# Kernel optimization log

Hardware: AMD Instinct MI355X
Metric: run time of the kernel (lower is better)

The kernel has to match this reference:

```python
import jax, jax.numpy as jnp
import numpy as np

WD, WH, WW = 1, 7, 7
N = WD * WH * WW  # 49 tokens per window
LN_EPS = 1e-5


def _make_rel_coords_table():
    rd = np.arange(-(WD - 1), WD, dtype=np.float32)
    rh = np.arange(-(WH - 1), WH, dtype=np.float32)
    rw = np.arange(-(WW - 1), WW, dtype=np.float32)
    g = np.stack(np.meshgrid(rd, rh, rw, indexing='ij'), axis=-1)  # (2wd-1,2wh-1,2ww-1,3)
    eps = 1e-6
    g = g / (np.array([WD, WH, WW], np.float32) - (1.0 - eps))
    g = g * 8.0
    g = np.sign(g) * np.log2(np.abs(g) + 1.0) / np.log2(8.0)
    return g[None].astype(np.float32)  # (1,2wd-1,2wh-1,2ww-1,3)


def _make_rel_pos_index():
    coords = np.stack(np.meshgrid(np.arange(WD), np.arange(WH), np.arange(WW), indexing='ij'))
    cf = coords.reshape(3, -1)  # (3,N)
    rel = cf[:, :, None] - cf[:, None, :]  # (3,N,N)
    rel = rel.transpose(1, 2, 0).astype(np.int64)
    rel[..., 0] += WD - 1
    rel[..., 1] += WH - 1
    rel[..., 2] += WW - 1
    rel[..., 0] *= (2 * WH - 1) * (2 * WW - 1)
    rel[..., 1] *= 2 * WW - 1
    return rel.sum(-1).astype(np.int32)  # (N,N)


def setup_inputs() -> dict:
    key = jax.random.key(0)
    ks = jax.random.split(key, 8)
    B, D, H, W, C = 4, 8, 56, 56, 256
    nh, hid = 8, 4 * C

    def init_w(k, shape, fan_in):
        return (jax.random.normal(k, shape, jnp.float32) / np.sqrt(fan_in)).astype(jnp.float32)

    inp = {
        'x': jax.random.normal(ks[0], (B, D, H, W, C), jnp.float32),
        'qkv_w': init_w(ks[1], (3 * C, C), C),
        'q_bias': jnp.zeros((C,), jnp.float32),
        'v_bias': jnp.zeros((C,), jnp.float32),
        'logit_scale': jnp.full((nh, 1, 1), np.log(10.0), jnp.float32),
        'cpb_w1': init_w(ks[2], (512, 3), 3),
        'cpb_b1': jnp.zeros((512,), jnp.float32),
        'cpb_w2': init_w(ks[3], (nh, 512), 512),
        'proj_w': init_w(ks[4], (C, C), C),
        'proj_b': jnp.zeros((C,), jnp.float32),
        'norm1_g': jnp.ones((C,), jnp.float32),
        'norm1_b': jnp.zeros((C,), jnp.float32),
        'fc1_w': init_w(ks[5], (hid, C), C),
        'fc1_b': jnp.zeros((hid,), jnp.float32),
        'fc2_w': init_w(ks[6], (C, hid), hid),
        'fc2_b': jnp.zeros((C,), jnp.float32),
        'norm2_g': jnp.ones((C,), jnp.float32),
        'norm2_b': jnp.zeros((C,), jnp.float32),
        'rel_coords_table': jnp.asarray(_make_rel_coords_table()),
        'rel_pos_index': jnp.asarray(_make_rel_pos_index()),
    }
    return inp


def _layernorm(x, g, b):
    mu = jnp.mean(x, axis=-1, keepdims=True)
    var = jnp.mean(jnp.square(x - mu), axis=-1, keepdims=True)
    return (x - mu) * jax.lax.rsqrt(var + LN_EPS) * g + b


def _l2norm(x):
    # F.normalize(dim=-1): x / max(||x||, 1e-12)
    n = jnp.sqrt(jnp.sum(jnp.square(x), axis=-1, keepdims=True))
    return x / jnp.maximum(n, 1e-12)


def _forward(x, qkv_w, q_bias, v_bias, logit_scale, cpb_w1, cpb_b1, cpb_w2,
             proj_w, proj_b, norm1_g, norm1_b, fc1_w, fc1_b, fc2_w, fc2_b,
             norm2_g, norm2_b, rel_coords_table, rel_pos_index):
    B, D, H, W, C = x.shape
    nh = logit_scale.shape[0]
    hd = C // nh

    # ---- window partition: (B,D,H,W,C) -> (B_, N, C)
    xw = x.reshape(B, D // WD, WD, H // WH, WH, W // WW, WW, C)
    xw = xw.transpose(0, 1, 3, 5, 2, 4, 6, 7).reshape(-1, N, C)
    Bw = xw.shape[0]

    # ---- qkv with (q_bias, 0, v_bias)
    qkv_bias = jnp.concatenate([q_bias, jnp.zeros_like(q_bias), v_bias])
    qkv = xw @ qkv_w.T + qkv_bias  # (Bw,N,3C)
    qkv = qkv.reshape(Bw, N, 3, nh, hd).transpose(2, 0, 3, 1, 4)
    q, k, v = qkv[0], qkv[1], qkv[2]  # (Bw,nh,N,hd)

    # ---- cosine attention with clamped learned logit scale
    attn = jnp.einsum('bhnd,bhmd->bhnm', _l2norm(q), _l2norm(k))
    scale = jnp.exp(jnp.minimum(logit_scale, jnp.float32(np.log(100.0))))  # (nh,1,1)
    attn = attn * scale

    # ---- CPB-MLP relative position bias
    t = rel_coords_table.reshape(-1, 3)
    hcpb = jax.nn.relu(t @ cpb_w1.T + cpb_b1)
    table = hcpb @ cpb_w2.T  # (T, nh)
    rpb = table[rel_pos_index.reshape(-1)].reshape(N, N, nh).transpose(2, 0, 1)
    rpb = 16.0 * jax.nn.sigmoid(rpb)
    attn = attn + rpb[None]

    attn = jax.nn.softmax(attn, axis=-1)
    out = jnp.einsum('bhnm,bhmd->bhnd', attn, v)
    out = out.transpose(0, 2, 1, 3).reshape(Bw, N, C)
    out = out @ proj_w.T + proj_b

    # ---- window reverse
    xr = out.reshape(B, D // WD, H // WH, W // WW, WD, WH, WW, C)
    xr = xr.transpose(0, 1, 4, 2, 5, 3, 6, 7).reshape(B, D, H, W, C)

    # ---- Swin-v2 post-norm residuals
    x = x + _layernorm(xr, norm1_g, norm1_b)
    h = jax.nn.gelu(x @ fc1_w.T + fc1_b, approximate=False)
    y = h @ fc2_w.T + fc2_b
    x = x + _layernorm(y, norm2_g, norm2_b)
    return x


def reference(x, qkv_w, q_bias, v_bias, logit_scale, cpb_w1, cpb_b1, cpb_w2,
              proj_w, proj_b, norm1_g, norm1_b, fc1_w, fc1_b, fc2_w, fc2_b,
              norm2_g, norm2_b, rel_coords_table, rel_pos_index):
    return _forward(x, qkv_w, q_bias, v_bias, logit_scale, cpb_w1, cpb_b1, cpb_w2,
                    proj_w, proj_b, norm1_g, norm1_b, fc1_w, fc1_b, fc2_w, fc2_b,
                    norm2_g, norm2_b, rel_coords_table, rel_pos_index)
```

## Files before the change

kernel.cpp:

```cpp
#include <hip/hip_runtime.h>
#include <hip/hip_bf16.h>

typedef __attribute__((ext_vector_type(8))) short short8_t;
typedef __attribute__((ext_vector_type(4))) float f32x4;

__device__ __forceinline__ float bf2f(unsigned short u) {
    return __uint_as_float(((unsigned)u) << 16);
}
__device__ __forceinline__ unsigned short f2bf(float f) {
    __hip_bfloat16 h = __float2bfloat16(f);
    return *reinterpret_cast<unsigned short*>(&h);
}

__device__ __forceinline__ float fast_gelu(float v) {
    float ax = fabsf(v) * 0.70710678118f;
    float t  = __builtin_amdgcn_rcpf(1.f + 0.3275911f * ax);
    float poly = t * (0.254829592f + t * (-0.284496736f + t * (1.421413741f
               + t * (-1.453152027f + t * 1.061405429f))));
    float e  = __expf(-ax * ax);
    float er = 1.f - poly * e;
    float s  = (v >= 0.f) ? er : -er;
    return 0.5f * v * (1.f + s);
}

__device__ __forceinline__ void async16(const unsigned short* g, unsigned short* l) {
    __builtin_amdgcn_global_load_lds(
        (const __attribute__((address_space(1))) unsigned int*)g,
        (__attribute__((address_space(3))) unsigned int*)l,
        16, 0, 0);
}

__device__ __forceinline__ int win_row_to_token(int r) {
    int wb = r / 49, n = r - wb * 49;
    int wq = wb & 7, hb = (wb >> 3) & 7, d = (wb >> 6) & 7, b = wb >> 9;
    int hh = n / 7, ww2 = n - hh * 7;
    return ((b * 8 + d) * 56 + hb * 7 + hh) * 56 + wq * 7 + ww2;
}

__global__ __launch_bounds__(256) void conv_kernel(
    const float* __restrict__ src, unsigned short* __restrict__ dst, int n4)
{
    int stride = gridDim.x * 256;
    for (int i = blockIdx.x * 256 + threadIdx.x; i < n4; i += stride) {
        float4 v = *reinterpret_cast<const float4*>(&src[(size_t)i * 4]);
        short4 o;
        o.x = (short)f2bf(v.x); o.y = (short)f2bf(v.y);
        o.z = (short)f2bf(v.z); o.w = (short)f2bf(v.w);
        *reinterpret_cast<short4*>(&dst[(size_t)i * 4]) = o;
    }
}

__global__ __launch_bounds__(256) void conv4_kernel(
    const float* __restrict__ s0, unsigned short* __restrict__ d0, int n0,
    const float* __restrict__ s1, unsigned short* __restrict__ d1, int n1,
    const float* __restrict__ s2, unsigned short* __restrict__ d2, int n2,
    const float* __restrict__ s3, unsigned short* __restrict__ d3, int n3)
{
    int stride = gridDim.x * 256;
    int total = n0 + n1 + n2 + n3;
    for (int i = blockIdx.x * 256 + threadIdx.x; i < total; i += stride) {
        const float* s; unsigned short* d; int j = i;
        if (j < n0) { s = s0; d = d0; }
        else if ((j -= n0) < n1) { s = s1; d = d1; }
        else if ((j -= n1) < n2) { s = s2; d = d2; }
        else { j -= n2; s = s3; d = d3; }
        float4 v = *reinterpret_cast<const float4*>(&s[(size_t)j * 4]);
        short4 o;
        o.x = (short)f2bf(v.x); o.y = (short)f2bf(v.y);
        o.z = (short)f2bf(v.z); o.w = (short)f2bf(v.w);
        *reinterpret_cast<short4*>(&d[(size_t)j * 4]) = o;
    }
}

__global__ __launch_bounds__(256) void prep_table_kernel(
    const float* __restrict__ w1, const float* __restrict__ b1,
    const float* __restrict__ w2, const float* __restrict__ tabin,
    float* __restrict__ tableg)
{
    const int i = blockIdx.x;
    const int t = threadIdx.x;
    const float c0 = tabin[i * 3], c1 = tabin[i * 3 + 1], c2 = tabin[i * 3 + 2];
    float part[8] = {0.f, 0.f, 0.f, 0.f, 0.f, 0.f, 0.f, 0.f};
    for (int j = t; j < 512; j += 256) {
        float hv = fmaxf(c0 * w1[j * 3] + c1 * w1[j * 3 + 1] + c2 * w1[j * 3 + 2] + b1[j], 0.f);
        #pragma unroll
        for (int h = 0; h < 8; ++h) part[h] += hv * w2[h * 512 + j];
    }
    #pragma unroll
    for (int h = 0; h < 8; ++h) {
        float v = part[h];
        v += __shfl_xor(v, 1);  v += __shfl_xor(v, 2);  v += __shfl_xor(v, 4);
        v += __shfl_xor(v, 8);  v += __shfl_xor(v, 16); v += __shfl_xor(v, 32);
        part[h] = v;
    }
    __shared__ float red[4][8];
    const int wv = t >> 6, lane = t & 63;
    if (lane == 0) {
        #pragma unroll
        for (int h = 0; h < 8; ++h) red[wv][h] = part[h];
    }
    __syncthreads();
    if (t < 8) tableg[i * 8 + t] = red[0][t] + red[1][t] + red[2][t] + red[3][t];
}

__global__ __launch_bounds__(256) void prep_expand_kernel(
    const float* __restrict__ logit_scale,
    const float* __restrict__ qb, const float* __restrict__ vb,
    const int* __restrict__ rpi, const float* __restrict__ tableg,
    float* __restrict__ scales, float* __restrict__ rpbf,
    float* __restrict__ qkvb)
{
    const int stride = gridDim.x * 256;
    const int gt = blockIdx.x * 256 + threadIdx.x;
    if (gt < 8) scales[gt] = expf(fminf(logit_scale[gt], 4.6051702f));
    for (int i = gt; i < 768; i += stride) {
        float o;
        if (i < 256) o = qb[i];
        else if (i < 512) o = 0.f;
        else o = vb[i - 512];
        qkvb[i] = o;
    }
    for (int e = gt; e < 32768; e += stride) {
        int h = e >> 12, rem = e & 4095;
        int mi = rem >> 10, ji = (rem >> 8) & 3;
        int r16 = (rem >> 4) & 15, g4 = (rem >> 2) & 3, r = rem & 3;
        int i = mi * 16 + g4 * 4 + r, j = ji * 16 + r16;
        float val = 0.f;
        if (i < 49 && j < 49) {
            float xv = tableg[rpi[i * 49 + j] * 8 + h];
            val = 16.f / (1.f + expf(-xv));
        }
        rpbf[e] = val;
    }
}

template<int ACT>
__global__ __launch_bounds__(512, 6) void gemm2_kernel(
    const unsigned short* __restrict__ A, const unsigned short* __restrict__ W,
    const float* __restrict__ bias, unsigned short* __restrict__ C,
    int M, int N, int K, int ntn)
{
    __shared__ unsigned short smem[24576];
    const int tid = threadIdx.x;
    const int lane = tid & 63, wv = tid >> 6;
    const int wr = wv >> 2, wc = wv & 3;
    const int nwg = gridDim.x;
    const int virt = (blockIdx.x & 7) * (nwg >> 3) + (blockIdx.x >> 3);
    const int bn = virt % ntn, bm = virt / ntn;
    const size_t arow0 = (size_t)bm * 128;
    const size_t brow0 = (size_t)bn * 128;
    const int r16 = lane & 15, g4 = lane >> 4;
    const int srow_l = lane >> 2;
    const int sgran  = (lane & 3) ^ ((srow_l >> 1) & 3);
    f32x4 acc[4][2] = {};

    auto STAGE = [&](int buf, int kt) {
        unsigned short* As = smem + buf * 8192;
        unsigned short* Bs = As + 4096;
        int row0 = wv * 16;
        async16(&A[(arow0 + row0 + srow_l) * (size_t)K + kt + sgran * 8], &As[row0 * 32]);
        async16(&W[(brow0 + row0 + srow_l) * (size_t)K + kt + sgran * 8], &Bs[row0 * 32]);
    };
    auto COMPUTE = [&](int buf) {
        unsigned short* As = smem + buf * 8192;
        unsigned short* Bs = As + 4096;
        short8_t af[4], bfr[2];
        const int gsw = g4 ^ ((r16 >> 1) & 3);
        #pragma unroll
        for (int m = 0; m < 4; ++m) {
            int row = wr * 64 + m * 16 + r16;
            af[m] = *reinterpret_cast<const short8_t*>(&As[row * 32 + gsw * 8]);
        }
        #pragma unroll
        for (int n = 0; n < 2; ++n) {
            int row = wc * 32 + n * 16 + r16;
            bfr[n] = *reinterpret_cast<const short8_t*>(&Bs[row * 32 + gsw * 8]);
        }
        #pragma unroll
        for (int m = 0; m < 4; ++m)
            #pragma unroll
            for (int n = 0; n < 2; ++n)
                acc[m][n] = __builtin_amdgcn_mfma_f32_16x16x32_bf16(af[m], bfr[n], acc[m][n], 0, 0, 0);
    };

    const int nk = K >> 5;
    STAGE(0, 0);
    STAGE(1, 32);
    int cb = 0;
    for (int ks = 0; ks < nk; ++ks) {
        if (ks == nk - 1) { asm volatile("s_waitcnt vmcnt(0)" ::: "memory"); }
        else              { asm volatile("s_waitcnt vmcnt(2)" ::: "memory"); }
        __builtin_amdgcn_sched_barrier(0);
        asm volatile("s_barrier" ::: "memory");
        if (ks + 2 < nk) {
            int sb = cb + 2; if (sb >= 3) sb -= 3;
            STAGE(sb, (ks + 2) << 5);
        }
        __builtin_amdgcn_sched_barrier(0);
        COMPUTE(cb);
        cb = (cb == 2) ? 0 : cb + 1;
    }
    __builtin_amdgcn_sched_barrier(0);
    asm volatile("s_barrier" ::: "memory");

    unsigned short* Cs = smem + wv * 2304;
    const int rbase = g4 * 4;
    const int srow = lane >> 2, scol = (lane & 3) * 8;
    const int gcol0 = bn * 128 + wc * 32;
    #pragma unroll
    for (int n = 0; n < 2; ++n) {
        float bv = bias[gcol0 + n * 16 + r16];
        #pragma unroll
        for (int m = 0; m < 4; ++m)
            #pragma unroll
            for (int r = 0; r < 4; ++r) {
                float v = acc[m][n][r] + bv;
                if (ACT == 1) v = fast_gelu(v);
                Cs[(m * 16 + rbase + r) * 36 + n * 16 + r16] = f2bf(v);
            }
    }
    #pragma unroll
    for (int pass = 0; pass < 4; ++pass) {
        int lr = pass * 16 + srow;
        int grow = bm * 128 + wr * 64 + lr;
        short8_t vv = *reinterpret_cast<const short8_t*>(&Cs[lr * 36 + scol]);
        *reinterpret_cast<short8_t*>(&C[(size_t)grow * N + gcol0 + scol]) = vv;
    }
}

template<int SCATTER, int OUT_F32>
__global__ __launch_bounds__(512) void gemm_ln_kernel(
    const unsigned short* __restrict__ A, const unsigned short* __restrict__ W,
    const float* __restrict__ bias, const unsigned short* __restrict__ resid,
    const float* __restrict__ gamma, const float* __restrict__ beta,
    void* __restrict__ Cv, int M, int K)
{
    __shared__ unsigned short smem[36864];
    const int tid = threadIdx.x;
    const int lane = tid & 63, wv = tid >> 6;
    const int wr = wv >> 2, wc = wv & 3;
    const int nwg = gridDim.x;
    const int bm = (blockIdx.x & 7) * (nwg >> 3) + (blockIdx.x >> 3);
    const size_t arow0 = (size_t)bm * 128;
    const int r16 = lane & 15, g4 = lane >> 4;
    const int srow_l = lane >> 2;
    const int sgran = (lane & 3) ^ ((srow_l >> 1) & 3);
    f32x4 acc[4][4] = {};

    auto STAGE = [&](int buf, int kt) {
        unsigned short* As = smem + buf * 12288;
        unsigned short* Bs = As + 4096;
        async16(&A[(arow0 + wv * 16 + srow_l) * (size_t)K + kt + sgran * 8],
                &As[(wv * 16) * 32]);
        #pragma unroll
        for (int i = 0; i < 2; ++i) {
            int row0 = wv * 32 + i * 16;
            async16(&W[(size_t)(row0 + srow_l) * K + kt + sgran * 8], &Bs[row0 * 32]);
        }
    };
    auto COMPUTE = [&](int buf) {
        unsigned short* As = smem + buf * 12288;
        unsigned short* Bs = As + 4096;
        short8_t af[4], bfr[4];
        const int gsw = g4 ^ ((r16 >> 1) & 3);
        #pragma unroll
        for (int m = 0; m < 4; ++m) {
            int row = wr * 64 + m * 16 + r16;
            af[m] = *reinterpret_cast<const short8_t*>(&As[row * 32 + gsw * 8]);
        }
        #pragma unroll
        for (int n = 0; n < 4; ++n) {
            int row = wc * 64 + n * 16 + r16;
            bfr[n] = *reinterpret_cast<const short8_t*>(&Bs[row * 32 + gsw * 8]);
        }
        #pragma unroll
        for (int m = 0; m < 4; ++m)
            #pragma unroll
            for (int n = 0; n < 4; ++n)
                acc[m][n] = __builtin_amdgcn_mfma_f32_16x16x32_bf16(af[m], bfr[n], acc[m][n], 0, 0, 0);
    };

    const int nk = K >> 5;
    STAGE(0, 0);
    STAGE(1, 32);
    int cb = 0;
    for (int ks = 0; ks < nk; ++ks) {
        if (ks == nk - 1) { asm volatile("s_waitcnt vmcnt(0)" ::: "memory"); }
        else              { asm volatile("s_waitcnt vmcnt(3)" ::: "memory"); }
        __builtin_amdgcn_sched_barrier(0);
        asm volatile("s_barrier" ::: "memory");
        if (ks + 2 < nk) {
            int sb = cb + 2; if (sb >= 3) sb -= 3;
            STAGE(sb, (ks + 2) << 5);
        }
        __builtin_amdgcn_sched_barrier(0);
        COMPUTE(cb);
        cb = (cb == 2) ? 0 : cb + 1;
    }
    __builtin_amdgcn_sched_barrier(0);
    asm volatile("s_barrier" ::: "memory");

    float bv[4];
    #pragma unroll
    for (int n = 0; n < 4; ++n) bv[n] = bias[wc * 64 + n * 16 + r16];
    float* psum  = reinterpret_cast<float*>(smem + 19456);
    float* psq   = psum + 512;
    float* stats = psq + 512;
    #pragma unroll
    for (int m = 0; m < 4; ++m) {
        #pragma unroll
        for (int r = 0; r < 4; ++r) {
            float s = 0.f, s2 = 0.f;
            #pragma unroll
            for (int n = 0; n < 4; ++n) {
                float v = acc[m][n][r] + bv[n];
                s += v; s2 += v * v;
            }
            s  += __shfl_xor(s, 1);  s  += __shfl_xor(s, 2);
            s  += __shfl_xor(s, 4);  s  += __shfl_xor(s, 8);
            s2 += __shfl_xor(s2, 1); s2 += __shfl_xor(s2, 2);
            s2 += __shfl_xor(s2, 4); s2 += __shfl_xor(s2, 8);
            if (r16 == 0) {
                int row = wr * 64 + m * 16 + g4 * 4 + r;
                psum[row * 4 + wc] = s;
                psq[row * 4 + wc]  = s2;
            }
        }
    }
    __syncthreads();
    if (tid < 128) {
        f32x4 a = *reinterpret_cast<const f32x4*>(&psum[tid * 4]);
        f32x4 b = *reinterpret_cast<const f32x4*>(&psq[tid * 4]);
        float mu  = (a[0] + a[1] + a[2] + a[3]) * 0.00390625f;
        float ex2 = (b[0] + b[1] + b[2] + b[3]) * 0.00390625f;
        stats[tid * 2]     = mu;
        stats[tid * 2 + 1] = rsqrtf(ex2 - mu * mu + 1e-5f);
    }
    __syncthreads();

    unsigned short* Cs = smem + wv * 2432;
    const int rbase = g4 * 4;
    const int srow = lane >> 3, scol = (lane & 7) * 8;
    const int gcol0 = wc * 64;
    f32x4 gm0 = *reinterpret_cast<const f32x4*>(&gamma[gcol0 + scol]);
    f32x4 gm1 = *reinterpret_cast<const f32x4*>(&gamma[gcol0 + scol + 4]);
    f32x4 bt0 = *reinterpret_cast<const f32x4*>(&beta[gcol0 + scol]);
    f32x4 bt1 = *reinterpret_cast<const f32x4*>(&beta[gcol0 + scol + 4]);
    #pragma unroll
    for (int p = 0; p < 2; ++p) {
        #pragma unroll
        for (int n = 0; n < 4; ++n)
            #pragma unroll
            for (int m2 = 0; m2 < 2; ++m2)
                #pragma unroll
                for (int r = 0; r < 4; ++r)
                    Cs[(m2 * 16 + rbase + r) * 76 + n * 16 + r16] =
                        f2bf(acc[p * 2 + m2][n][r] + bv[n]);
        #pragma unroll
        for (int rr = 0; rr < 4; ++rr) {
            int lr = rr * 8 + srow;
            int lrow = wr * 64 + p * 32 + lr;
            int grow = bm * 128 + lrow;
            size_t orow = SCATTER ? (size_t)win_row_to_token(grow) : (size_t)grow;
            float mu  = stats[lrow * 2];
            float inv = stats[lrow * 2 + 1];
            short8_t cv = *reinterpret_cast<const short8_t*>(&Cs[lr * 76 + scol]);
            short8_t rv = *reinterpret_cast<const short8_t*>(&resid[orow * 256 + gcol0 + scol]);
            float o[8];
            #pragma unroll
            for (int e = 0; e < 8; ++e) {
                float g = (e < 4) ? gm0[e] : gm1[e - 4];
                float bb = (e < 4) ? bt0[e] : bt1[e - 4];
                o[e] = bf2f((unsigned short)rv[e])
                     + (bf2f((unsigned short)cv[e]) - mu) * inv * g + bb;
            }
            if (OUT_F32) {
                float* outp = (float*)Cv + orow * 256 + gcol0 + scol;
                f32x4 o0, o1;
                #pragma unroll
                for (int e = 0; e < 4; ++e) { o0[e] = o[e]; o1[e] = o[e + 4]; }
                *reinterpret_cast<f32x4*>(outp)     = o0;
                *reinterpret_cast<f32x4*>(outp + 4) = o1;
            } else {
                unsigned short* outp = (unsigned short*)Cv + orow * 256 + gcol0 + scol;
                short8_t ov;
                #pragma unroll
                for (int e = 0; e < 8; ++e) ov[e] = (short)f2bf(o[e]);
                *reinterpret_cast<short8_t*>(outp) = ov;
            }
        }
    }
}

__global__ __launch_bounds__(64) void attn_kernel(
    const unsigned short* __restrict__ qkv, const float* __restrict__ scales,
    const float* __restrict__ rpbf, unsigned short* __restrict__ out)
{
    constexpr int PO = 0;
    constexpr int VO = 4608;
    __shared__ unsigned short lds[6912];

    const int blk = blockIdx.x;
    const int h = blk & 7, wb = blk >> 3;
    const int lane = threadIdx.x;
    const int r16 = lane & 15, g4 = lane >> 4;

    const int wq = wb & 7, hb = (wb >> 3) & 7, dd = (wb >> 6) & 7, bb2 = wb >> 9;
    const int tok_base = ((bb2 * 8 + dd) * 56 + hb * 7) * 56 + wq * 7;
    const float sc = scales[h];

    {
        short8_t z = {};
        int d = lane >> 1, j0 = 48 + (lane & 1) * 8;
        *reinterpret_cast<short8_t*>(&lds[VO + d * 72 + j0]) = z;
    }
    for (int c = lane; c < 196; c += 64) {
        int j = c >> 2, gi = c & 3;
        int tok = tok_base + (j / 7) * 56 + (j % 7);
        short8_t raw = *reinterpret_cast<const short8_t*>(
            qkv + (size_t)tok * 768 + 512 + h * 32 + gi * 8);
        #pragma unroll
        for (int e = 0; e < 8; ++e)
            lds[VO + (gi * 8 + e) * 72 + j] = (unsigned short)raw[e];
    }

    short8_t qf[4], kf[4];
    #pragma unroll
    for (int sel = 0; sel < 2; ++sel) {
        #pragma unroll
        for (int mi = 0; mi < 4; ++mi) {
            int row = mi * 16 + r16;
            int tok = tok_base + (row / 7) * 56 + (row % 7);
            short8_t raw = *reinterpret_cast<const short8_t*>(
                qkv + (size_t)tok * 768 + sel * 256 + h * 32 + g4 * 8);
            float f[8]; float ss = 0.f;
            #pragma unroll
            for (int e = 0; e < 8; ++e) { f[e] = bf2f((unsigned short)raw[e]); ss += f[e] * f[e]; }
            ss += __shfl_xor(ss, 16); ss += __shfl_xor(ss, 32);
            float inv = 1.f / fmaxf(sqrtf(ss), 1e-12f);
            if (sel == 0) inv *= sc;
            short8_t o;
            #pragma unroll
            for (int e = 0; e < 8; ++e) o[e] = (short)f2bf(f[e] * inv);
            if (sel == 0) qf[mi] = o; else kf[mi] = o;
        }
    }
    __syncthreads();

    f32x4 acc[4][4] = {};
    __builtin_amdgcn_s_setprio(1);
    #pragma unroll
    for (int mi = 0; mi < 4; ++mi)
        #pragma unroll
        for (int ji = 0; ji < 4; ++ji)
            acc[mi][ji] = __builtin_amdgcn_mfma_f32_16x16x32_bf16(qf[mi], kf[ji], acc[mi][ji], 0, 0, 0);
    __builtin_amdgcn_s_setprio(0);

    const float* rbf = rpbf + h * 4096 + r16 * 16 + g4 * 4;
    f32x4 rbv[4][4];
    #pragma unroll
    for (int mi = 0; mi < 4; ++mi)
        #pragma unroll
        for (int ji = 0; ji < 4; ++ji)
            rbv[mi][ji] = *reinterpret_cast<const f32x4*>(&rbf[(mi * 4 + ji) * 256]);

    #pragma unroll
    for (int mi = 0; mi < 4; ++mi) {
        #pragma unroll
        for (int r = 0; r < 4; ++r) {
            int i = mi * 16 + g4 * 4 + r;
            float s[4]; float m = -1e30f;
            #pragma unroll
            for (int ji = 0; ji < 4; ++ji) {
                int j = ji * 16 + r16;
                float v = acc[mi][ji][r] + rbv[mi][ji][r];
                s[ji] = (j < 49) ? v : -1e30f;
                m = fmaxf(m, s[ji]);
            }
            m = fmaxf(m, __shfl_xor(m, 1)); m = fmaxf(m, __shfl_xor(m, 2));
            m = fmaxf(m, __shfl_xor(m, 4)); m = fmaxf(m, __shfl_xor(m, 8));
            float p[4]; float sum = 0.f;
            #pragma unroll
            for (int ji = 0; ji < 4; ++ji) {
                p[ji] = (s[ji] > -1e29f) ? __expf(s[ji] - m) : 0.f;
                sum += p[ji];
            }
            sum += __shfl_xor(sum, 1); sum += __shfl_xor(sum, 2);
            sum += __shfl_xor(sum, 4); sum += __shfl_xor(sum, 8);
            float rinv = 1.f / sum;
            #pragma unroll
            for (int ji = 0; ji < 4; ++ji) {
                int j = ji * 16 + r16;
                lds[PO + i * 72 + j] = f2bf(p[ji] * rinv);
            }
        }
    }
    __syncthreads();

    f32x4 acc2[4][2] = {};
    __builtin_amdgcn_s_setprio(1);
    #pragma unroll
    for (int ks = 0; ks < 2; ++ks) {
        short8_t pf[4], vf[2];
        int ko = ks * 32 + g4 * 8;
        #pragma unroll
        for (int mi = 0; mi < 4; ++mi)
            pf[mi] = *reinterpret_cast<const short8_t*>(&lds[PO + (mi * 16 + r16) * 72 + ko]);
        #pragma unroll
        for (int ni = 0; ni < 2; ++ni)
            vf[ni] = *reinterpret_cast<const short8_t*>(&lds[VO + (ni * 16 + r16) * 72 + ko]);
        #pragma unroll
        for (int mi = 0; mi < 4; ++mi)
            #pragma unroll
            for (int ni = 0; ni < 2; ++ni)
                acc2[mi][ni] = __builtin_amdgcn_mfma_f32_16x16x32_bf16(pf[mi], vf[ni], acc2[mi][ni], 0, 0, 0);
    }
    __builtin_amdgcn_s_setprio(0);

    #pragma unroll
    for (int mi = 0; mi < 4; ++mi)
        #pragma unroll
        for (int r = 0; r < 4; ++r) {
            int i = mi * 16 + g4 * 4 + r;
            if (i < 49) {
                size_t ob = (size_t)(wb * 49 + i) * 256 + h * 32;
                out[ob + r16]      = f2bf(acc2[mi][0][r]);
                out[ob + 16 + r16] = f2bf(acc2[mi][1][r]);
            }
        }
}

extern "C" void kernel_launch(void* const* d_in, const int* in_sizes, int n_in,
                              void* d_out, int out_size, void* d_ws, size_t ws_size,
                              hipStream_t stream) {
    const float* x      = (const float*)d_in[0];
    const float* qkv_w  = (const float*)d_in[1];
    const float* q_bias = (const float*)d_in[2];
    const float* v_bias = (const float*)d_in[3];
    const float* lscale = (const float*)d_in[4];
    const float* cpb_w1 = (const float*)d_in[5];
    const float* cpb_b1 = (const float*)d_in[6];
    const float* cpb_w2 = (const float*)d_in[7];
    const float* proj_w = (const float*)d_in[8];
    const float* proj_b = (const float*)d_in[9];
    const float* n1g    = (const float*)d_in[10];
    const float* n1b    = (const float*)d_in[11];
    const float* fc1_w  = (const float*)d_in[12];
    const float* fc1_b  = (const float*)d_in[13];
    const float* fc2_w  = (const float*)d_in[14];
    const float* fc2_b  = (const float*)d_in[15];
    const float* n2g    = (const float*)d_in[16];
    const float* n2b    = (const float*)d_in[17];
    const float* rct    = (const float*)d_in[18];
    const int*   rpi    = (const int*)d_in[19];

    char* ws = (char*)d_ws;
    unsigned short* qkv    = (unsigned short*)(ws);
    unsigned short* hbuf   = (unsigned short*)(ws);
    unsigned short* attn_o = (unsigned short*)(ws + 154140672);
    unsigned short* xb     = (unsigned short*)(ws + 205520896);
    unsigned short* x1     = (unsigned short*)(ws + 205520896);
    unsigned short* wqkv   = (unsigned short*)(ws + 308281344);
    unsigned short* wproj  = (unsigned short*)(ws + 308674560);
    unsigned short* wfc1   = (unsigned short*)(ws + 308805632);
    unsigned short* wfc2   = (unsigned short*)(ws + 309329920);
    float*          rpbf   = (float*)(ws + 309854208);
    float*          scales = (float*)(ws + 310378496);
    float*          qkvb   = (float*)(ws + 310378528);
    float*          tableg = (float*)(ws + 310381600);

    const int M = 100352;

    conv_kernel<<<2048, 256, 0, stream>>>(x, xb, 25690112 / 4);
    conv4_kernel<<<768, 256, 0, stream>>>(qkv_w, wqkv, 49152,
                                          proj_w, wproj, 16384,
                                          fc1_w, wfc1, 65536,
                                          fc2_w, wfc2, 65536);
    prep_table_kernel<<<169, 256, 0, stream>>>(cpb_w1, cpb_b1, cpb_w2, rct, tableg);
    prep_expand_kernel<<<128, 256, 0, stream>>>(lscale, q_bias, v_bias, rpi, tableg,
                                                scales, rpbf, qkvb);
    gemm2_kernel<0><<<4704, 512, 0, stream>>>(xb, wqkv, qkvb, qkv, M, 768, 256, 6);
    attn_kernel<<<16384, 64, 0, stream>>>(qkv, scales, rpbf, attn_o);
    gemm_ln_kernel<1, 0><<<784, 512, 0, stream>>>(attn_o, wproj, proj_b, xb, n1g, n1b,
                                                  x1, M, 256);
    gemm2_kernel<1><<<6272, 512, 0, stream>>>(x1, wfc1, fc1_b, hbuf, M, 1024, 256, 8);
    gemm_ln_kernel<0, 1><<<784, 512, 0, stream>>>(hbuf, wfc2, fc2_b, x1, n2g, n2b,
                                                  d_out, M, 1024);
}
```

Before: 437.0 us.

## Fuse fc1+GELU and fc2+LayerNorm into a single MLP kernel per row tile

Replaces the separate fc1 GEMM and fc2+LN kernels with one kernel where each 128-row block computes all eight 128-column fc1 tiles, applies GELU, and writes the hidden activations. It then runs fc2 with residual LayerNorm on those same rows. This removes a launch and is meant to improve L2 locality, since H rows are re-read right after being written by the same block. The trade-off is that fc1 now runs on only 784 blocks instead of 6272, which lowers parallelism and adds serialization inside each block.

```diff
diff --git a/kernel.cpp b/kernel.cpp
--- a/kernel.cpp
+++ b/kernel.cpp
@@ -388,6 +388,241 @@
                 for (int e = 0; e < 8; ++e) ov[e] = (short)f2bf(o[e]);
                 *reinterpret_cast<short8_t*>(outp) = ov;
             }
+        }
+    }
+}
+
+__global__ __launch_bounds__(512) void mlp2_kernel(
+    const unsigned short* __restrict__ A,
+    const unsigned short* __restrict__ W1,
+    const float* __restrict__ b1,
+    unsigned short* __restrict__ H,
+    const unsigned short* __restrict__ W2,
+    const float* __restrict__ b2,
+    const float* __restrict__ gamma, const float* __restrict__ beta,
+    float* __restrict__ out, int M)
+{
+    __shared__ unsigned short smem[24576];
+    const int tid = threadIdx.x;
+    const int lane = tid & 63, wv = tid >> 6;
+    const int wr = wv >> 2, wc = wv & 3;
+    const int nwg = gridDim.x;
+    const int bm = (blockIdx.x & 7) * (nwg >> 3) + (blockIdx.x >> 3);
+    const size_t arow0 = (size_t)bm * 128;
+    const int r16 = lane & 15, g4 = lane >> 4;
+    const int srow_l = lane >> 2;
+    const int sgran = (lane & 3) ^ ((srow_l >> 1) & 3);
+    const int gsw = g4 ^ ((r16 >> 1) & 3);
+
+    for (int bn = 0; bn < 8; ++bn) {
+        asm volatile("s_waitcnt lgkmcnt(0)" ::: "memory");
+        __builtin_amdgcn_sched_barrier(0);
+        asm volatile("s_barrier" ::: "memory");
+
+        f32x4 acc[4][2] = {};
+        auto STAGE1 = [&](int buf, int kt) {
+            unsigned short* As = smem + buf * 8192;
+            unsigned short* Bs = As + 4096;
+            int row0 = wv * 16;
+            async16(&A[(arow0 + row0 + srow_l) * 256 + kt + sgran * 8], &As[row0 * 32]);
+            async16(&W1[(size_t)(bn * 128 + row0 + srow_l) * 256 + kt + sgran * 8], &Bs[row0 * 32]);
+        };
+        auto COMPUTE1 = [&](int buf) {
+            unsigned short* As = smem + buf * 8192;
+            unsigned short* Bs = As + 4096;
+            short8_t af[4], bfr[2];
+            #pragma unroll
+            for (int m = 0; m < 4; ++m) {
+                int row = wr * 64 + m * 16 + r16;
+                af[m] = *reinterpret_cast<const short8_t*>(&As[row * 32 + gsw * 8]);
+            }
+            #pragma unroll
+            for (int n = 0; n < 2; ++n) {
+                int row = wc * 32 + n * 16 + r16;
+                bfr[n] = *reinterpret_cast<const short8_t*>(&Bs[row * 32 + gsw * 8]);
+            }
+            #pragma unroll
+            for (int m = 0; m < 4; ++m)
+                #pragma unroll
+                for (int n = 0; n < 2; ++n)
+                    acc[m][n] = __builtin_amdgcn_mfma_f32_16x16x32_bf16(af[m], bfr[n], acc[m][n], 0, 0, 0);
+        };
+
+        STAGE1(0, 0);
+        STAGE1(1, 32);
+        int cb = 0;
+        for (int ks = 0; ks < 8; ++ks) {
+            if (ks == 7) { asm volatile("s_waitcnt vmcnt(0)" ::: "memory"); }
+            else         { asm volatile("s_waitcnt vmcnt(2)" ::: "memory"); }
+            __builtin_amdgcn_sched_barrier(0);
+            asm volatile("s_barrier" ::: "memory");
+            if (ks + 2 < 8) {
+                int sb = cb + 2; if (sb >= 3) sb -= 3;
+                STAGE1(sb, (ks + 2) << 5);
+            }
+            __builtin_amdgcn_sched_barrier(0);
+            COMPUTE1(cb);
+            cb = (cb == 2) ? 0 : cb + 1;
+        }
+        __builtin_amdgcn_sched_barrier(0);
+        asm volatile("s_barrier" ::: "memory");
+
+        unsigned short* Cs = smem + wv * 2304;
+        const int rbase = g4 * 4;
+        const int srow = lane >> 2, scol = (lane & 3) * 8;
+        const int gcol0 = bn * 128 + wc * 32;
+        #pragma unroll
+        for (int n = 0; n < 2; ++n) {
+            float bv = b1[gcol0 + n * 16 + r16];
+            #pragma unroll
+            for (int m = 0; m < 4; ++m)
+                #pragma unroll
+                for (int r = 0; r < 4; ++r)
+                    Cs[(m * 16 + rbase + r) * 36 + n * 16 + r16] =
+                        f2bf(fast_gelu(acc[m][n][r] + bv));
+        }
+        #pragma unroll
+        for (int pass = 0; pass < 4; ++pass) {
+            int lr = pass * 16 + srow;
+            int grow = bm * 128 + wr * 64 + lr;
+            short8_t vv = *reinterpret_cast<const short8_t*>(&Cs[lr * 36 + scol]);
+            *reinterpret_cast<short8_t*>(&H[(size_t)grow * 1024 + gcol0 + scol]) = vv;
+        }
+    }
+
+    asm volatile("s_waitcnt vmcnt(0) lgkmcnt(0)" ::: "memory");
+    __builtin_amdgcn_sched_barrier(0);
+    asm volatile("s_barrier" ::: "memory");
+
+    f32x4 acc2[4][4] = {};
+    auto STAGE2 = [&](int buf, int kt) {
+        unsigned short* As = smem + buf * 12288;
+        unsigned short* Bs = As + 4096;
+        async16(&H[(arow0 + wv * 16 + srow_l) * 1024 + kt + sgran * 8],
+                &As[(wv * 16) * 32]);
+        #pragma unroll
+        for (int i = 0; i < 2; ++i) {
+            int row0 = wv * 32 + i * 16;
+            async16(&W2[(size_t)(row0 + srow_l) * 1024 + kt + sgran * 8], &Bs[row0 * 32]);
+        }
+    };
+    auto COMPUTE2 = [&](int buf) {
+        unsigned short* As = smem + buf * 12288;
+        unsigned short* Bs = As + 4096;
+        short8_t af[4], bfr[4];
+        #pragma unroll
+        for (int m = 0; m < 4; ++m) {
+            int row = wr * 64 + m * 16 + r16;
+            af[m] = *reinterpret_cast<const short8_t*>(&As[row * 32 + gsw * 8]);
+        }
+        #pragma unroll
+        for (int n = 0; n < 4; ++n) {
+            int row = wc * 64 + n * 16 + r16;
+            bfr[n] = *reinterpret_cast<const short8_t*>(&Bs[row * 32 + gsw * 8]);
+        }
+        #pragma unroll
+        for (int m = 0; m < 4; ++m)
+            #pragma unroll
+            for (int n = 0; n < 4; ++n)
+                acc2[m][n] = __builtin_amdgcn_mfma_f32_16x16x32_bf16(af[m], bfr[n], acc2[m][n], 0, 0, 0);
+    };
+
+    STAGE2(0, 0);
+    STAGE2(1, 32);
+    int cur = 0;
+    for (int ks = 0; ks < 32; ++ks) {
+        if (ks == 31) { asm volatile("s_waitcnt vmcnt(0)" ::: "memory"); }
+        else          { asm volatile("s_waitcnt vmcnt(3)" ::: "memory"); }
+        __builtin_amdgcn_sched_barrier(0);
+        asm volatile("s_barrier" ::: "memory");
+        COMPUTE2(cur);
+        __builtin_amdgcn_sched_barrier(0);
+        asm volatile("s_barrier" ::: "memory");
+        if (ks + 2 < 32) STAGE2(cur, (ks + 2) << 5);
+        cur ^= 1;
+    }
+    __builtin_amdgcn_sched_barrier(0);
+    asm volatile("s_barrier" ::: "memory");
+
+    float bv2[4];
+    #pragma unroll
+    for (int n = 0; n < 4; ++n) bv2[n] = b2[wc * 64 + n * 16 + r16];
+    float* psum  = reinterpret_cast<float*>(smem + 19456);
+    float* psq   = psum + 512;
+    float* stats = psq + 512;
+    #pragma unroll
+    for (int m = 0; m < 4; ++m) {
+        #pragma unroll
+        for (int r = 0; r < 4; ++r) {
+            float s = 0.f, s2 = 0.f;
+            #pragma unroll
+            for (int n = 0; n < 4; ++n) {
+                float v = acc2[m][n][r] + bv2[n];
+                s += v; s2 += v * v;
+            }
+            s  += __shfl_xor(s, 1);  s  += __shfl_xor(s, 2);
+            s  += __shfl_xor(s, 4);  s  += __shfl_xor(s, 8);
+            s2 += __shfl_xor(s2, 1); s2 += __shfl_xor(s2, 2);
+            s2 += __shfl_xor(s2, 4); s2 += __shfl_xor(s2, 8);
+            if (r16 == 0) {
+                int row = wr * 64 + m * 16 + g4 * 4 + r;
+                psum[row * 4 + wc] = s;
+                psq[row * 4 + wc]  = s2;
+            }
+        }
+    }
+    __syncthreads();
+    if (tid < 128) {
+        f32x4 a = *reinterpret_cast<const f32x4*>(&psum[tid * 4]);
+        f32x4 b = *reinterpret_cast<const f32x4*>(&psq[tid * 4]);
+        float mu  = (a[0] + a[1] + a[2] + a[3]) * 0.00390625f;
+        float ex2 = (b[0] + b[1] + b[2] + b[3]) * 0.00390625f;
+        stats[tid * 2]     = mu;
+        stats[tid * 2 + 1] = rsqrtf(ex2 - mu * mu + 1e-5f);
+    }
+    __syncthreads();
+
+    unsigned short* Cs = smem + wv * 2432;
+    const int rbase = g4 * 4;
+    const int srow = lane >> 3, scol = (lane & 7) * 8;
+    const int gcol0 = wc * 64;
+    f32x4 gm0 = *reinterpret_cast<const f32x4*>(&gamma[gcol0 + scol]);
+    f32x4 gm1 = *reinterpret_cast<const f32x4*>(&gamma[gcol0 + scol + 4]);
+    f32x4 bt0 = *reinterpret_cast<const f32x4*>(&beta[gcol0 + scol]);
+    f32x4 bt1 = *reinterpret_cast<const f32x4*>(&beta[gcol0 + scol + 4]);
+    #pragma unroll
+    for (int p = 0; p < 2; ++p) {
+        #pragma unroll
+        for (int n = 0; n < 4; ++n)
+            #pragma unroll
+            for (int m2 = 0; m2 < 2; ++m2)
+                #pragma unroll
+                for (int r = 0; r < 4; ++r)
+                    Cs[(m2 * 16 + rbase + r) * 76 + n * 16 + r16] =
+                        f2bf(acc2[p * 2 + m2][n][r] + bv2[n]);
+        #pragma unroll
+        for (int rr = 0; rr < 4; ++rr) {
+            int lr = rr * 8 + srow;
+            int lrow = wr * 64 + p * 32 + lr;
+            int grow = bm * 128 + lrow;
+            float mu  = stats[lrow * 2];
+            float inv = stats[lrow * 2 + 1];
+            short8_t cv = *reinterpret_cast<const short8_t*>(&Cs[lr * 76 + scol]);
+            short8_t rv = *reinterpret_cast<const short8_t*>(&A[(size_t)grow * 256 + gcol0 + scol]);
+            float o[8];
+            #pragma unroll
+            for (int e = 0; e < 8; ++e) {
+                float g = (e < 4) ? gm0[e] : gm1[e - 4];
+                float bb = (e < 4) ? bt0[e] : bt1[e - 4];
+                o[e] = bf2f((unsigned short)rv[e])
+                     + (bf2f((unsigned short)cv[e]) - mu) * inv * g + bb;
+            }
+            float* outp = out + (size_t)grow * 256 + gcol0 + scol;
+            f32x4 o0, o1;
+            #pragma unroll
+            for (int e = 0; e < 4; ++e) { o0[e] = o[e]; o1[e] = o[e + 4]; }
+            *reinterpret_cast<f32x4*>(outp)     = o0;
+            *reinterpret_cast<f32x4*>(outp + 4) = o1;
         }
     }
 }
@@ -583,7 +818,6 @@
     attn_kernel<<<16384, 64, 0, stream>>>(qkv, scales, rpbf, attn_o);
     gemm_ln_kernel<1, 0><<<784, 512, 0, stream>>>(attn_o, wproj, proj_b, xb, n1g, n1b,
                                                   x1, M, 256);
-    gemm2_kernel<1><<<6272, 512, 0, stream>>>(x1, wfc1, fc1_b, hbuf, M, 1024, 256, 8);
-    gemm_ln_kernel<0, 1><<<784, 512, 0, stream>>>(hbuf, wfc2, fc2_b, x1, n2g, n2b,
-                                                  d_out, M, 1024);
-}
+    mlp2_kernel<<<784, 512, 0, stream>>>(x1, wfc1, fc1_b, hbuf, wfc2, fc2_b,
+                                         n2g, n2b, (float*)d_out, M);
+}
```

New measurement: 447.6 us. 1.02x slower.
